# Optimization experiments

Measured on AMD Instinct MI355X. Metric: run time of the kernel, lower is better.

## Reference

```python
import jax, jax.numpy as jnp
import numpy as np
from jax import lax

C_IN = 256
C_OUT = 256
KS = 3


def _conv(x, w, b):
    # x: [B,C,H,W], w: [O,I,kh,kw] -> NCHW 'SAME' conv, stride 1
    y = lax.conv_general_dilated(x, w, window_strides=(1, 1), padding='SAME',
                                 dimension_numbers=('NCHW', 'OIHW', 'NCHW'))
    return y + b[None, :, None, None]


def setup_inputs() -> dict:
    key = jax.random.key(0)
    ks = jax.random.split(key, 7)
    B, H, W = 2, 64, 64
    fan = C_IN * KS * KS
    lim = float(np.sqrt(6.0 / (fan + C_OUT * KS * KS)))  # xavier uniform
    return {
        'x': jax.random.normal(ks[0], (B, C_IN, H, W), jnp.float32),
        'ref_x': jax.random.normal(ks[1], (B, C_IN, H, W), jnp.float32),
        'conv1_w': jax.random.uniform(ks[2], (C_OUT, C_IN, KS, KS), jnp.float32, -lim, lim),
        'conv1_b': jnp.zeros((C_OUT,), jnp.float32),
        'conv2_w': jax.random.uniform(ks[3], (C_OUT, C_IN, KS, KS), jnp.float32, -lim, lim),
        'conv2_b': jnp.zeros((C_OUT,), jnp.float32),
        'gamma': jnp.array([0.5], jnp.float32),
    }


def reference(x, ref_x, conv1_w, conv1_b, conv2_w, conv2_b, gamma):
    B, Cin, H, W = x.shape
    HW = H * W
    x_f = jax.nn.relu(_conv(x, conv1_w, conv1_b)).reshape(B, C_OUT, HW)        # [B,C,HW]
    r_f = jax.nn.relu(_conv(ref_x, conv1_w, conv1_b))                          # [B,C,H,W]
    r_f = r_f.transpose(0, 2, 3, 1).reshape(B, HW, C_OUT)                      # [B,HW,C]
    corr = jnp.einsum('bnc,bcm->bnm', r_f, x_f)                                # [B,HW,HW]
    corr = jax.nn.softmax(corr, axis=1)                                        # softmax over ref positions
    ref_c2 = jax.nn.relu(_conv(x, conv2_w, conv2_b)).reshape(B, C_OUT, HW)     # [B,C,HW]
    A = jnp.einsum('bcn,bnm->bcm', ref_c2, corr).reshape(x.shape)              # [B,C,H,W]
    return A * gamma[0] + x
```

## Files before the change

### kernel.cpp

```cpp
#include <hip/hip_runtime.h>
#include <hip/hip_bf16.h>

#define B_ 2
#define C_ 256
#define H_ 64
#define W_ 64
#define N_ 4096

typedef short bf16x8 __attribute__((ext_vector_type(8)));
typedef _Float16 f16x8 __attribute__((ext_vector_type(8)));
typedef float f32x4 __attribute__((ext_vector_type(4)));
typedef float f32x16 __attribute__((ext_vector_type(16)));

static __device__ __forceinline__ unsigned short f2bf(float f) {
    union { float f; unsigned u; } uf; uf.f = f;
    unsigned r = uf.u + 0x7fffu + ((uf.u >> 16) & 1u);
    return (unsigned short)(r >> 16);
}
static __device__ __forceinline__ unsigned short f2h_u(float f) {
    union { _Float16 h; unsigned short u; } c; c.h = (_Float16)f; return c.u;
}

static __device__ __forceinline__ void gload16(const void* g, void* l) {
    __builtin_amdgcn_global_load_lds(
        (const __attribute__((address_space(1))) unsigned int*)g,
        (__attribute__((address_space(3))) unsigned int*)l, 16, 0, 0);
}

__global__ __launch_bounds__(256) void cvt_x_k(const float* __restrict__ x,
                                               const float* __restrict__ ref_x,
                                               unsigned short* __restrict__ xtx,
                                               unsigned short* __restrict__ xtr)
{
    __shared__ unsigned short t[64][72];
    const int pt = blockIdx.x, ct = blockIdx.y;
    const int which = blockIdx.z >> 1, b = blockIdx.z & 1;
    const float* in = which ? ref_x : x;
    unsigned short* out = which ? xtr : xtx;
    const int a = threadIdx.x & 63, r = threadIdx.x >> 6;
    #pragma unroll
    for (int i = 0; i < 16; ++i) {
        int c = i * 4 + r;
        t[c][a] = f2h_u(in[((size_t)(b * C_ + ct * 64 + c) << 12) + pt * 64 + a]);
    }
    __syncthreads();
    #pragma unroll
    for (int i = 0; i < 16; ++i) {
        int p = i * 4 + r;
        out[((size_t)(b * N_ + pt * 64 + p) << 8) + ct * 64 + a] = t[a][p];
    }
}

__global__ __launch_bounds__(256) void cvt_w_k(const float* __restrict__ w1,
                                               const float* __restrict__ w2,
                                               unsigned short* __restrict__ wh1,
                                               unsigned short* __restrict__ wh2)
{
    int g = blockIdx.x;
    const float* w = (g < 2304) ? w1 : w2;
    unsigned short* wh = (g < 2304) ? wh1 : wh2;
    int i = (g % 2304) * 256 + threadIdx.x;
    int ci = i & 255, co = (i >> 8) & 255, tap = i >> 16;
    wh[i] = f2h_u(w[((size_t)(co * 256 + ci)) * 9 + tap]);
}

__global__ __launch_bounds__(256) void conv_mfma_k(
    const unsigned short* __restrict__ xtx, const unsigned short* __restrict__ xtr,
    const unsigned short* __restrict__ w1h, const unsigned short* __restrict__ w2h,
    const float* __restrict__ b1, const float* __restrict__ b2,
    unsigned short* __restrict__ f1x, unsigned short* __restrict__ f1r,
    unsigned short* __restrict__ f2)
{
    __shared__ unsigned short As[9 * 64 * 32];
    __shared__ unsigned short Bs[6 * 66 * 32];
    const int tid = threadIdx.x;
    const int pt  = blockIdx.x;
    const int cot = blockIdx.y;
    const int cid = blockIdx.z >> 1;
    const int b   = blockIdx.z & 1;

    const unsigned short* xt = (cid == 1) ? xtr : xtx;
    const unsigned short* wt = (cid == 2) ? w2h : w1h;
    const float* bias = (cid == 2) ? b2 : b1;
    unsigned short* out = (cid == 0) ? f1x : (cid == 1) ? f1r : f2;
    const int trans = (cid != 2);

    const int lane = tid & 63, wid = tid >> 6;
    const int rl32 = lane & 31, l5 = lane >> 5;
    const int r0 = pt * 4;

    f32x16 acc[2][2];
    #pragma unroll
    for (int fm = 0; fm < 2; ++fm)
        #pragma unroll
        for (int fn = 0; fn < 2; ++fn)
            #pragma unroll
            for (int e = 0; e < 16; ++e) acc[fm][fn][e] = 0.f;

    for (int k0 = 0; k0 < C_; k0 += 32) {
        #pragma unroll
        for (int tap = 0; tap < 9; ++tap) {
            gload16(wt + ((size_t)(tap * C_ + cot * 64 + wid * 16 + (lane >> 2)) << 8)
                       + k0 + (lane & 3) * 8,
                    &As[tap * 2048 + wid * 512 + lane * 8]);
        }
        #pragma unroll
        for (int j = 0; j < 7; ++j) {
            int it = tid + j * 256;
            if (it < 1584) {
                int col = it / 24;
                int rem = it - col * 24;
                int row = rem >> 2, qb = rem & 3;
                int h = r0 + row - 1, c = col - 1;
                float4 v; v.x = 0.f; v.y = 0.f; v.z = 0.f; v.w = 0.f;
                if (h >= 0 && h < 64 && c >= 0 && c < 64)
                    v = *(const float4*)(xt + ((size_t)(b * N_ + h * 64 + c) << 8) + k0 + qb * 8);
                int chunk = qb ^ ((col >> 1) & 3);
                *(float4*)&Bs[(row * 66 + col) * 32 + chunk * 8] = v;
            }
        }
        __syncthreads();

        #pragma unroll
        for (int tap = 0; tap < 9; ++tap) {
            const int kh = tap / 3, kw = tap % 3;
            f16x8 a[2][2], bb[2][2];
            #pragma unroll
            for (int fm = 0; fm < 2; ++fm)
                #pragma unroll
                for (int kk = 0; kk < 2; ++kk)
                    a[fm][kk] = *(const f16x8*)&As[(tap * 64 + fm * 32 + rl32) * 32 + kk * 16 + l5 * 8];
            #pragma unroll
            for (int fn = 0; fn < 2; ++fn) {
                const int colB = fn * 32 + rl32 + kw;
                const int sw = ((rl32 + kw) >> 1) & 3;
                #pragma unroll
                for (int kk = 0; kk < 2; ++kk) {
                    const int kc = kk * 2 + l5;
                    bb[fn][kk] = *(const f16x8*)&Bs[((wid + kh) * 66 + colB) * 32 + (kc ^ sw) * 8];
                }
            }
            #pragma unroll
            for (int fm = 0; fm < 2; ++fm)
                #pragma unroll
                for (int fn = 0; fn < 2; ++fn)
                    #pragma unroll
                    for (int kk = 0; kk < 2; ++kk)
                        acc[fm][fn] = __builtin_amdgcn_mfma_f32_32x32x16_f16(
                            a[fm][kk], bb[fn][kk], acc[fm][fn], 0, 0, 0);
        }
        __syncthreads();
    }

    const int prow = r0 + wid;
    #pragma unroll
    for (int fm = 0; fm < 2; ++fm)
        #pragma unroll
        for (int fn = 0; fn < 2; ++fn) {
            const int pos = prow * 64 + fn * 32 + rl32;
            #pragma unroll
            for (int g = 0; g < 4; ++g) {
                const int co0 = cot * 64 + fm * 32 + g * 8 + l5 * 4;
                if (trans) {
                    unsigned short pk[4];
                    #pragma unroll
                    for (int rr = 0; rr < 4; ++rr)
                        pk[rr] = f2bf(fmaxf(acc[fm][fn][g * 4 + rr] + bias[co0 + rr], 0.f));
                    uint2 u;
                    u.x = (unsigned)pk[0] | ((unsigned)pk[1] << 16);
                    u.y = (unsigned)pk[2] | ((unsigned)pk[3] << 16);
                    *(uint2*)&out[((size_t)(b * N_ + pos) << 8) + co0] = u;
                } else {
                    #pragma unroll
                    for (int rr = 0; rr < 4; ++rr)
                        out[((size_t)(b * C_ + co0 + rr) << 12) + pos] =
                            f2bf(fmaxf(acc[fm][fn][g * 4 + rr] + bias[co0 + rr], 0.f));
                }
            }
        }
}

__global__ __launch_bounds__(256) void gemm_corr_k(
    const unsigned short* __restrict__ f1x, const unsigned short* __restrict__ f1r,
    float* __restrict__ corr)
{
    __shared__ alignas(16) unsigned short As[128 * 32];
    __shared__ alignas(16) unsigned short Bs[128 * 32];
    const int tid = threadIdx.x;
    const int tn = blockIdx.x, tm = blockIdx.y, b = blockIdx.z;

    const unsigned short* Ab = f1x + ((size_t)b * N_ + (size_t)tm * 128) * C_;
    const unsigned short* Bb = f1r + ((size_t)b * N_ + (size_t)tn * 128) * C_;

    const int wid = tid >> 6, lane = tid & 63;
    const int wr = wid >> 1, wc = wid & 1;
    const int rl32 = lane & 31, l5 = lane >> 5;
    const int srow = wid * 32 + (lane >> 2), sq = lane & 3;

    f32x16 acc[2][2];
    #pragma unroll
    for (int fm = 0; fm < 2; ++fm)
        #pragma unroll
        for (int fn = 0; fn < 2; ++fn)
            #pragma unroll
            for (int e = 0; e < 16; ++e) acc[fm][fn][e] = 0.f;

    for (int k0 = 0; k0 < C_; k0 += 32) {
        gload16(&Ab[(size_t)srow * C_ + k0 + sq * 8],        &As[srow * 32 + sq * 8]);
        gload16(&Ab[(size_t)(srow + 16) * C_ + k0 + sq * 8], &As[(srow + 16) * 32 + sq * 8]);
        gload16(&Bb[(size_t)srow * C_ + k0 + sq * 8],        &Bs[srow * 32 + sq * 8]);
        gload16(&Bb[(size_t)(srow + 16) * C_ + k0 + sq * 8], &Bs[(srow + 16) * 32 + sq * 8]);
        __syncthreads();
        bf16x8 a[2][2], bb[2][2];
        #pragma unroll
        for (int fm = 0; fm < 2; ++fm)
            #pragma unroll
            for (int kk = 0; kk < 2; ++kk)
                a[fm][kk] = *(const bf16x8*)&As[(wr * 64 + fm * 32 + rl32) * 32 + kk * 16 + l5 * 8];
        #pragma unroll
        for (int fn = 0; fn < 2; ++fn)
            #pragma unroll
            for (int kk = 0; kk < 2; ++kk)
                bb[fn][kk] = *(const bf16x8*)&Bs[(wc * 64 + fn * 32 + rl32) * 32 + kk * 16 + l5 * 8];
        #pragma unroll
        for (int fm = 0; fm < 2; ++fm)
            #pragma unroll
            for (int fn = 0; fn < 2; ++fn)
                #pragma unroll
                for (int kk = 0; kk < 2; ++kk)
                    acc[fm][fn] = __builtin_amdgcn_mfma_f32_32x32x16_bf16(
                        a[fm][kk], bb[fn][kk], acc[fm][fn], 0, 0, 0);
        __syncthreads();
    }

    #pragma unroll
    for (int fm = 0; fm < 2; ++fm)
        #pragma unroll
        for (int fn = 0; fn < 2; ++fn) {
            const int n = tn * 128 + wc * 64 + fn * 32 + rl32;
            #pragma unroll
            for (int g = 0; g < 4; ++g) {
                const int m0 = tm * 128 + wr * 64 + fm * 32 + g * 8 + l5 * 4;
                #pragma unroll
                for (int rr = 0; rr < 4; ++rr)
                    corr[((size_t)b * N_ + m0 + rr) * N_ + n] = acc[fm][fn][g * 4 + rr];
            }
        }
}

__global__ __launch_bounds__(256) void softmax_rows_k(float* __restrict__ corr)
{
    __shared__ float red[4];
    const int m = blockIdx.x, b = blockIdx.y;
    float* row = corr + ((size_t)b * N_ + m) * N_;
    float4* row4 = (float4*)row;
    const int tid = threadIdx.x;
    const int wid = tid >> 6, lane = tid & 63;

    float4 v[4];
    float mx = -3.0e38f;
    #pragma unroll
    for (int j = 0; j < 4; ++j) {
        v[j] = row4[tid + j * 256];
        mx = fmaxf(mx, fmaxf(fmaxf(v[j].x, v[j].y), fmaxf(v[j].z, v[j].w)));
    }
    #pragma unroll
    for (int off = 32; off; off >>= 1) mx = fmaxf(mx, __shfl_xor(mx, off));
    if (lane == 0) red[wid] = mx;
    __syncthreads();
    mx = fmaxf(fmaxf(red[0], red[1]), fmaxf(red[2], red[3]));
    __syncthreads();

    float s = 0.f;
    #pragma unroll
    for (int j = 0; j < 4; ++j) {
        v[j].x = __expf(v[j].x - mx);
        v[j].y = __expf(v[j].y - mx);
        v[j].z = __expf(v[j].z - mx);
        v[j].w = __expf(v[j].w - mx);
        s += v[j].x + v[j].y + v[j].z + v[j].w;
    }
    #pragma unroll
    for (int off = 32; off; off >>= 1) s += __shfl_xor(s, off);
    if (lane == 0) red[wid] = s;
    __syncthreads();
    s = red[0] + red[1] + red[2] + red[3];
    const float inv = 1.f / s;

    unsigned short* rb = (unsigned short*)row;
    #pragma unroll
    for (int j = 0; j < 4; ++j) {
        uint2 u;
        u.x = (unsigned)f2bf(v[j].x * inv) | ((unsigned)f2bf(v[j].y * inv) << 16);
        u.y = (unsigned)f2bf(v[j].z * inv) | ((unsigned)f2bf(v[j].w * inv) << 16);
        *(uint2*)&rb[4 * (tid + j * 256)] = u;
    }
}

__global__ __launch_bounds__(512) void gemm_out_k(
    const unsigned short* __restrict__ f2, float* __restrict__ corr)
{
    __shared__ alignas(16) unsigned short As[128 * 32];
    __shared__ alignas(16) unsigned short Bs[128 * 32];
    const int tid = threadIdx.x;
    const int tm = blockIdx.x;
    const int tc = blockIdx.y >> 2;
    const int s  = blockIdx.y & 3;
    const int b  = blockIdx.z;

    const unsigned short* Ab = f2 + ((size_t)b * C_ + (size_t)tc * 128) * N_;
    const unsigned short* Bb = (const unsigned short*)corr
                             + ((size_t)b * N_ + (size_t)tm * 128) * 8192;

    const int wid = tid >> 6, lane = tid & 63;
    const int wc = wid >> 2, wm = wid & 3;
    const int rl = lane & 15, q = lane >> 4;
    const int srow = wid * 16 + (lane >> 2), sq = lane & 3;
    const int nbase = s * 1024;

    f32x4 acc[4][2];
    #pragma unroll
    for (int mi = 0; mi < 4; ++mi)
        #pragma unroll
        for (int ni = 0; ni < 2; ++ni)
            #pragma unroll
            for (int e = 0; e < 4; ++e) acc[mi][ni][e] = 0.f;

    for (int kk = 0; kk < 32; ++kk) {
        const int k0 = nbase + kk * 32;
        gload16(&Ab[(size_t)srow * N_ + k0 + sq * 8],   &As[srow * 32 + sq * 8]);
        gload16(&Bb[(size_t)srow * 8192 + k0 + sq * 8], &Bs[srow * 32 + sq * 8]);
        __syncthreads();
        bf16x8 a[4], bb[2];
        #pragma unroll
        for (int mi = 0; mi < 4; ++mi)
            a[mi] = *(const bf16x8*)&As[(wc * 64 + mi * 16 + rl) * 32 + q * 8];
        #pragma unroll
        for (int ni = 0; ni < 2; ++ni)
            bb[ni] = *(const bf16x8*)&Bs[(wm * 32 + ni * 16 + rl) * 32 + q * 8];
        #pragma unroll
        for (int mi = 0; mi < 4; ++mi)
            #pragma unroll
            for (int ni = 0; ni < 2; ++ni)
                acc[mi][ni] = __builtin_amdgcn_mfma_f32_16x16x32_bf16(a[mi], bb[ni], acc[mi][ni], 0, 0, 0);
        __syncthreads();
    }

    #pragma unroll
    for (int mi = 0; mi < 4; ++mi)
        #pragma unroll
        for (int ni = 0; ni < 2; ++ni)
            #pragma unroll
            for (int rr = 0; rr < 4; ++rr) {
                int c = tc * 128 + wc * 64 + mi * 16 + q * 4 + rr;
                int m = tm * 128 + wm * 32 + ni * 16 + rl;
                size_t e = (((size_t)(s * 2 + b) * C_ + c) << 12) + m;
                corr[(e >> 11) * 4096 + 2048 + (e & 2047)] = acc[mi][ni][rr];
            }
}

__global__ __launch_bounds__(256) void reduce_k(
    const float* __restrict__ corr, const float* __restrict__ x,
    const float* __restrict__ gamma, float* __restrict__ out)
{
    const float g = gamma[0];
    size_t i = (size_t)blockIdx.x * 256 + threadIdx.x;
    size_t idx = i << 2;
    float4 sum; sum.x = 0.f; sum.y = 0.f; sum.z = 0.f; sum.w = 0.f;
    #pragma unroll
    for (int sp = 0; sp < 4; ++sp) {
        size_t e = (size_t)sp * 2097152 + idx;
        float4 v = *(const float4*)&corr[(e >> 11) * 4096 + 2048 + (e & 2047)];
        sum.x += v.x; sum.y += v.y; sum.z += v.z; sum.w += v.w;
    }
    float4 xv = ((const float4*)x)[i];
    float4 o;
    o.x = sum.x * g + xv.x;
    o.y = sum.y * g + xv.y;
    o.z = sum.z * g + xv.z;
    o.w = sum.w * g + xv.w;
    ((float4*)out)[i] = o;
}

extern "C" void kernel_launch(void* const* d_in, const int* in_sizes, int n_in,
                              void* d_out, int out_size, void* d_ws, size_t ws_size,
                              hipStream_t stream) {
    const float* x     = (const float*)d_in[0];
    const float* ref_x = (const float*)d_in[1];
    const float* w1    = (const float*)d_in[2];
    const float* b1    = (const float*)d_in[3];
    const float* w2    = (const float*)d_in[4];
    const float* b2    = (const float*)d_in[5];
    const float* gamma = (const float*)d_in[6];
    float* out = (float*)d_out;

    char* ws = (char*)d_ws;
    size_t off = 0;
    auto nxt = [&](size_t bytes) {
        char* p = ws + off;
        off += (bytes + 255) & ~(size_t)255;
        return p;
    };
    unsigned short* f1x = (unsigned short*)nxt((size_t)B_ * N_ * C_ * 2);
    unsigned short* f1r = (unsigned short*)nxt((size_t)B_ * N_ * C_ * 2);
    unsigned short* f2  = (unsigned short*)nxt((size_t)B_ * N_ * C_ * 2);
    unsigned short* xtx = (unsigned short*)nxt((size_t)B_ * N_ * C_ * 2);
    unsigned short* xtr = (unsigned short*)nxt((size_t)B_ * N_ * C_ * 2);
    unsigned short* w1h = (unsigned short*)nxt((size_t)9 * C_ * C_ * 2);
    unsigned short* w2h = (unsigned short*)nxt((size_t)9 * C_ * C_ * 2);
    float* corr = (float*)nxt((size_t)B_ * N_ * N_ * 4);

    cvt_x_k<<<dim3(64, 4, 4), 256, 0, stream>>>(x, ref_x, xtx, xtr);
    cvt_w_k<<<4608, 256, 0, stream>>>(w1, w2, w1h, w2h);

    conv_mfma_k<<<dim3(16, 4, 6), 256, 0, stream>>>(xtx, xtr, w1h, w2h, b1, b2,
                                                    f1x, f1r, f2);

    gemm_corr_k<<<dim3(32, 32, B_), 256, 0, stream>>>(f1x, f1r, corr);
    softmax_rows_k<<<dim3(N_, B_), 256, 0, stream>>>(corr);
    gemm_out_k<<<dim3(32, 8, B_), 512, 0, stream>>>(f2, corr);
    reduce_k<<<2048, 256, 0, stream>>>(corr, x, gamma, out);
}
```

Baseline: 163.6 us.

## Use k-chunk-major LDS layouts so MFMA fragment reads are conflict-free

Reorganizes shared-memory tiles in the conv, correlation GEMM and output GEMM kernels so each 16-byte k-chunk is stored contiguously across rows (chunk-major), replacing row-major 32-element rows and the XOR swizzle. Global-to-LDS load thread mappings are remapped to match, so consecutive lanes write consecutive LDS slots while fragment reads by lanes stepping along rows also hit consecutive addresses. The goal is to remove LDS bank conflicts on ds_read_b128 fragment loads. Global loads now have less contiguous per-wavefront access (rows stride across lanes), which could reduce coalescing.

```diff
diff --git a/kernel.cpp b/kernel.cpp
--- a/kernel.cpp
+++ b/kernel.cpp
@@ -71,8 +71,8 @@
     unsigned short* __restrict__ f1x, unsigned short* __restrict__ f1r,
     unsigned short* __restrict__ f2)
 {
-    __shared__ unsigned short As[9 * 64 * 32];
-    __shared__ unsigned short Bs[6 * 66 * 32];
+    __shared__ unsigned short As[9 * 256 * 8];
+    __shared__ unsigned short Bs[1584 * 8];
     const int tid = threadIdx.x;
     const int pt  = blockIdx.x;
     const int cot = blockIdx.y;
@@ -89,6 +89,9 @@
     const int rl32 = lane & 31, l5 = lane >> 5;
     const int r0 = pt * 4;
 
+    const int a_co = ((tid >> 7) << 5) | (tid & 31);
+    const int a_q  = (tid >> 5) & 3;
+
     f32x16 acc[2][2];
     #pragma unroll
     for (int fm = 0; fm < 2; ++fm)
@@ -100,23 +103,20 @@
     for (int k0 = 0; k0 < C_; k0 += 32) {
         #pragma unroll
         for (int tap = 0; tap < 9; ++tap) {
-            gload16(wt + ((size_t)(tap * C_ + cot * 64 + wid * 16 + (lane >> 2)) << 8)
-                       + k0 + (lane & 3) * 8,
-                    &As[tap * 2048 + wid * 512 + lane * 8]);
+            gload16(wt + ((size_t)(tap * C_ + cot * 64 + a_co) << 8) + k0 + a_q * 8,
+                    &As[(tap * 256 + tid) * 8]);
         }
         #pragma unroll
         for (int j = 0; j < 7; ++j) {
             int it = tid + j * 256;
             if (it < 1584) {
-                int col = it / 24;
-                int rem = it - col * 24;
-                int row = rem >> 2, qb = rem & 3;
+                int g = it / 66, col = it - g * 66;
+                int row = g >> 2, kc = g & 3;
                 int h = r0 + row - 1, c = col - 1;
                 float4 v; v.x = 0.f; v.y = 0.f; v.z = 0.f; v.w = 0.f;
                 if (h >= 0 && h < 64 && c >= 0 && c < 64)
-                    v = *(const float4*)(xt + ((size_t)(b * N_ + h * 64 + c) << 8) + k0 + qb * 8);
-                int chunk = qb ^ ((col >> 1) & 3);
-                *(float4*)&Bs[(row * 66 + col) * 32 + chunk * 8] = v;
+                    v = *(const float4*)(xt + ((size_t)(b * N_ + h * 64 + c) << 8) + k0 + kc * 8);
+                *(float4*)&Bs[it * 8] = v;
             }
         }
         __syncthreads();
@@ -129,17 +129,13 @@
             for (int fm = 0; fm < 2; ++fm)
                 #pragma unroll
                 for (int kk = 0; kk < 2; ++kk)
-                    a[fm][kk] = *(const f16x8*)&As[(tap * 64 + fm * 32 + rl32) * 32 + kk * 16 + l5 * 8];
-            #pragma unroll
-            for (int fn = 0; fn < 2; ++fn) {
-                const int colB = fn * 32 + rl32 + kw;
-                const int sw = ((rl32 + kw) >> 1) & 3;
+                    a[fm][kk] = *(const f16x8*)&As[(tap * 256 + fm * 128 + (kk * 2 + l5) * 32 + rl32) * 8];
+            #pragma unroll
+            for (int fn = 0; fn < 2; ++fn)
                 #pragma unroll
-                for (int kk = 0; kk < 2; ++kk) {
-                    const int kc = kk * 2 + l5;
-                    bb[fn][kk] = *(const f16x8*)&Bs[((wid + kh) * 66 + colB) * 32 + (kc ^ sw) * 8];
-                }
-            }
+                for (int kk = 0; kk < 2; ++kk)
+                    bb[fn][kk] = *(const f16x8*)&Bs[(((wid + kh) * 4 + kk * 2 + l5) * 66
+                                                    + fn * 32 + rl32 + kw) * 8];
             #pragma unroll
             for (int fm = 0; fm < 2; ++fm)
                 #pragma unroll
@@ -184,8 +180,8 @@
     const unsigned short* __restrict__ f1x, const unsigned short* __restrict__ f1r,
     float* __restrict__ corr)
 {
-    __shared__ alignas(16) unsigned short As[128 * 32];
-    __shared__ alignas(16) unsigned short Bs[128 * 32];
+    __shared__ alignas(16) unsigned short As[512 * 8];
+    __shared__ alignas(16) unsigned short Bs[512 * 8];
     const int tid = threadIdx.x;
     const int tn = blockIdx.x, tm = blockIdx.y, b = blockIdx.z;
 
@@ -195,7 +191,10 @@
     const int wid = tid >> 6, lane = tid & 63;
     const int wr = wid >> 1, wc = wid & 1;
     const int rl32 = lane & 31, l5 = lane >> 5;
-    const int srow = wid * 32 + (lane >> 2), sq = lane & 3;
+
+    const int r0s = ((tid >> 7) << 5) | (tid & 31), q0s = (tid >> 5) & 3;
+    const int s1 = tid + 256;
+    const int r1s = ((s1 >> 7) << 5) | (s1 & 31), q1s = (s1 >> 5) & 3;
 
     f32x16 acc[2][2];
     #pragma unroll
@@ -206,22 +205,22 @@
             for (int e = 0; e < 16; ++e) acc[fm][fn][e] = 0.f;
 
     for (int k0 = 0; k0 < C_; k0 += 32) {
-        gload16(&Ab[(size_t)srow * C_ + k0 + sq * 8],        &As[srow * 32 + sq * 8]);
-        gload16(&Ab[(size_t)(srow + 16) * C_ + k0 + sq * 8], &As[(srow + 16) * 32 + sq * 8]);
-        gload16(&Bb[(size_t)srow * C_ + k0 + sq * 8],        &Bs[srow * 32 + sq * 8]);
-        gload16(&Bb[(size_t)(srow + 16) * C_ + k0 + sq * 8], &Bs[(srow + 16) * 32 + sq * 8]);
+        gload16(&Ab[(size_t)r0s * C_ + k0 + q0s * 8], &As[tid * 8]);
+        gload16(&Ab[(size_t)r1s * C_ + k0 + q1s * 8], &As[s1 * 8]);
+        gload16(&Bb[(size_t)r0s * C_ + k0 + q0s * 8], &Bs[tid * 8]);
+        gload16(&Bb[(size_t)r1s * C_ + k0 + q1s * 8], &Bs[s1 * 8]);
         __syncthreads();
         bf16x8 a[2][2], bb[2][2];
         #pragma unroll
         for (int fm = 0; fm < 2; ++fm)
             #pragma unroll
             for (int kk = 0; kk < 2; ++kk)
-                a[fm][kk] = *(const bf16x8*)&As[(wr * 64 + fm * 32 + rl32) * 32 + kk * 16 + l5 * 8];
+                a[fm][kk] = *(const bf16x8*)&As[((wr * 2 + fm) * 128 + (kk * 2 + l5) * 32 + rl32) * 8];
         #pragma unroll
         for (int fn = 0; fn < 2; ++fn)
             #pragma unroll
             for (int kk = 0; kk < 2; ++kk)
-                bb[fn][kk] = *(const bf16x8*)&Bs[(wc * 64 + fn * 32 + rl32) * 32 + kk * 16 + l5 * 8];
+                bb[fn][kk] = *(const bf16x8*)&Bs[((wc * 2 + fn) * 128 + (kk * 2 + l5) * 32 + rl32) * 8];
         #pragma unroll
         for (int fm = 0; fm < 2; ++fm)
             #pragma unroll
@@ -300,8 +299,8 @@
 __global__ __launch_bounds__(512) void gemm_out_k(
     const unsigned short* __restrict__ f2, float* __restrict__ corr)
 {
-    __shared__ alignas(16) unsigned short As[128 * 32];
-    __shared__ alignas(16) unsigned short Bs[128 * 32];
+    __shared__ alignas(16) unsigned short As[512 * 8];
+    __shared__ alignas(16) unsigned short Bs[512 * 8];
     const int tid = threadIdx.x;
     const int tm = blockIdx.x;
     const int tc = blockIdx.y >> 2;
@@ -315,8 +314,10 @@
     const int wid = tid >> 6, lane = tid & 63;
     const int wc = wid >> 2, wm = wid & 3;
     const int rl = lane & 15, q = lane >> 4;
-    const int srow = wid * 16 + (lane >> 2), sq = lane & 3;
     const int nbase = s * 1024;
+
+    const int srow = ((tid >> 6) << 4) | (tid & 15);
+    const int sq = (tid >> 4) & 3;
 
     f32x4 acc[4][2];
     #pragma unroll
@@ -328,16 +329,16 @@
 
     for (int kk = 0; kk < 32; ++kk) {
         const int k0 = nbase + kk * 32;
-        gload16(&Ab[(size_t)srow * N_ + k0 + sq * 8],   &As[srow * 32 + sq * 8]);
-        gload16(&Bb[(size_t)srow * 8192 + k0 + sq * 8], &Bs[srow * 32 + sq * 8]);
+        gload16(&Ab[(size_t)srow * N_ + k0 + sq * 8],   &As[tid * 8]);
+        gload16(&Bb[(size_t)srow * 8192 + k0 + sq * 8], &Bs[tid * 8]);
         __syncthreads();
         bf16x8 a[4], bb[2];
         #pragma unroll
         for (int mi = 0; mi < 4; ++mi)
-            a[mi] = *(const bf16x8*)&As[(wc * 64 + mi * 16 + rl) * 32 + q * 8];
+            a[mi] = *(const bf16x8*)&As[((wc * 4 + mi) * 64 + q * 16 + rl) * 8];
         #pragma unroll
         for (int ni = 0; ni < 2; ++ni)
-            bb[ni] = *(const bf16x8*)&Bs[(wm * 32 + ni * 16 + rl) * 32 + q * 8];
+            bb[ni] = *(const bf16x8*)&Bs[((wm * 2 + ni) * 64 + q * 16 + rl) * 8];
         #pragma unroll
         for (int mi = 0; mi < 4; ++mi)
             #pragma unroll
```

Measured after the change: 179.1 us. 9.4% more time.
